# Optimization experiments

Hardware: AMD Instinct MI355X
Metric: run time of the kernel (lower is better)

Reference implementation:

```python
import jax, jax.numpy as jnp
import numpy as np

# Per-sample token counts per octree depth layer (full octree, depth 1..5)
LENS = (8, 64, 512, 4096, 32768)
OFFS = np.concatenate([[0], np.cumsum(LENS)]).astype(int)
CONV = (1, 1, 1, 4, 8)  # conv stride/kernel per layer: basic x3, half-conv (2^(3-1)), single-conv (2^3)
B, E = 8, 256
NUM_VOCAB, RES, SDIM = 16, 32, 3
S = int(OFFS[-1])  # 37448


def setup_inputs() -> dict:
    key = jax.random.key(0)
    ks = jax.random.split(key, 16)
    value = jax.random.randint(ks[0], (B, S), 1, NUM_VOCAB + 1)
    # depth: fixed sorted octree pattern, same for every sample
    depth_row = np.concatenate([np.full(l, d + 1, dtype=np.int64) for d, l in enumerate(LENS)])
    depth = jnp.broadcast_to(jnp.asarray(depth_row), (B, S))
    position = jax.random.randint(ks[1], (B, S, SDIM), 1, 2 * RES)
    sc = 0.02
    val_emb = (jax.random.normal(ks[2], (5, NUM_VOCAB + 1, E)) * sc).at[:, 0].set(0.0)
    dep_emb = (jax.random.normal(ks[3], (5, RES + 1, E)) * sc).at[:, 0].set(0.0)
    pos_emb = (jax.random.normal(ks[4], (5, SDIM, 2 * RES, E)) * sc).at[:, :, 0].set(0.0)
    conv4_w = jax.random.normal(ks[5], (E, E, 4)) * sc
    conv4_b = jax.random.normal(ks[6], (E,)) * sc
    conv8_w = jax.random.normal(ks[7], (E, E, 8)) * sc
    conv8_b = jax.random.normal(ks[8], (E,)) * sc
    return {"value": value, "depth": depth, "position": position,
            "val_emb": val_emb, "dep_emb": dep_emb, "pos_emb": pos_emb,
            "conv4_w": conv4_w, "conv4_b": conv4_b, "conv8_w": conv8_w, "conv8_b": conv8_b}


def _embed(v, d, p, ve, de, pe):
    # sum of value, depth, and per-axis spatial embeddings  [B, L, E]
    return ve[v] + de[d] + pe[0][p[:, :, 0]] + pe[1][p[:, :, 1]] + pe[2][p[:, :, 2]]


def _conv(x, w, b, s):
    # Conv1d(kernel=stride=s) == blockwise GEMM over non-overlapping windows
    Bb, L, Ee = x.shape
    xr = x.reshape(Bb, L // s, s, Ee)
    return jnp.einsum('blki,oik->blo', xr, w) + b


def reference(value, depth, position, val_emb, dep_emb, pos_emb, conv4_w, conv4_b, conv8_w, conv8_b):
    convs = {3: (conv4_w, conv4_b), 4: (conv8_w, conv8_b)}
    outs = []
    for li in range(5):
        s0, s1 = int(OFFS[li]), int(OFFS[li + 1])
        x = _embed(value[:, s0:s1], depth[:, s0:s1], position[:, s0:s1],
                   val_emb[li], dep_emb[li], pos_emb[li])
        if CONV[li] > 1:
            w, b = convs[li]
            x = _conv(x, w, b, CONV[li])
        outs.append(x)
    # all samples share the depth layout -> equal lengths, pad_sequence is a no-op concat
    return jnp.concatenate(outs, axis=1)  # [B, 5704, E]
```

## Files before the change

kernel.cpp:

```cpp
#include <hip/hip_runtime.h>
#include <hip/hip_bf16.h>

#define S_TOT 37448
#define OUT_ROWS 5704
#define EDIM 256
#define BATCH 8

typedef __attribute__((ext_vector_type(8))) short short8;
typedef __attribute__((ext_vector_type(4))) float f32x4;
typedef __attribute__((ext_vector_type(4))) unsigned int u32x4;

__device__ __forceinline__ short f2b(float f) {
    unsigned u = __builtin_bit_cast(unsigned, f);
    unsigned r = (u + 0x7fffu + ((u >> 16) & 1u)) >> 16;
    return (short)r;
}
__device__ __forceinline__ float b2f(short s) {
    unsigned u = ((unsigned)(unsigned short)s) << 16;
    return __builtin_bit_cast(float, u);
}

__device__ __forceinline__ void embed8f(const float* ve, const float* de,
                                        const float* q0, const float* q1, const float* q2,
                                        float* s) {
#pragma unroll
    for (int h = 0; h < 2; ++h) {
        f32x4 a = *(const f32x4*)(ve + h * 4);
        f32x4 b = *(const f32x4*)(de + h * 4);
        f32x4 c = *(const f32x4*)(q0 + h * 4);
        f32x4 d = *(const f32x4*)(q1 + h * 4);
        f32x4 e = *(const f32x4*)(q2 + h * 4);
#pragma unroll
        for (int j = 0; j < 4; ++j)
            s[h * 4 + j] = a[j] + b[j] + c[j] + d[j] + e[j];
    }
}

__device__ __forceinline__ void acc_bf8(float* a, short8 s) {
    u32x4 u = __builtin_bit_cast(u32x4, s);
#pragma unroll
    for (int j = 0; j < 4; ++j) {
        a[2 * j]     += __builtin_bit_cast(float, u[j] << 16);
        a[2 * j + 1] += __builtin_bit_cast(float, u[j] & 0xffff0000u);
    }
}

template <int S>
__device__ __forceinline__ void transform_body(const float* __restrict__ w,
                                               short* __restrict__ dst, int bid, int tid) {
    int idx = bid * 256 + tid;
    int l  = idx & 63;
    int nf = (idx >> 6) & 15;
    int kb = idx >> 10;
    int o = nf * 16 + (l & 15);
    int kap0 = kb * 32 + ((l >> 4) << 3);
    short8 r;
#pragma unroll
    for (int j = 0; j < 8; ++j) {
        int kap = kap0 + j;
        int kpos = kap >> 8;
        int i = kap & 255;
        r[j] = f2b(w[(o * 256 + i) * S + kpos]);
    }
    *(short8*)(dst + idx * 8) = r;
}

__global__ __launch_bounds__(256) void transform_both(
        const float* __restrict__ w4, const float* __restrict__ w8,
        short* __restrict__ wt4, short* __restrict__ wt8) {
    int bid = blockIdx.x, tid = threadIdx.x;
    if (bid < 128) transform_body<4>(w4, wt4, bid, tid);
    else           transform_body<8>(w8, wt8, bid - 128, tid);
}

template <int S>
__device__ __forceinline__ void precompute_body(
        const float* __restrict__ val_emb, const float* __restrict__ dep_emb,
        const float* __restrict__ pos_emb, const short* __restrict__ wt2,
        short* __restrict__ P, int bid, int tid, short* As) {
    constexpr int LI = (S == 4) ? 3 : 4;
    const int lane = tid & 63;
    const int wid = tid >> 6;
    const int wave_m = wid >> 1;
    const int wave_n = wid & 1;
    const int k  = bid >> 2;
    const int mt = bid & 3;

    f32x4 acc[2][8];
#pragma unroll
    for (int i = 0; i < 2; ++i)
#pragma unroll
        for (int j = 0; j < 8; ++j) acc[i][j] = (f32x4){0.f, 0.f, 0.f, 0.f};

    const int tk = tid >> 5;
    const int f0 = (tid & 31) * 8;
    const float* dep = dep_emb + (LI * 33 + LI + 1) * 256;

#pragma unroll
    for (int m8 = 0; m8 < 8; ++m8) {
        int m = m8 * 8 + tk;
        int R = mt * 64 + m;
        short8 r;
        if (R < 17) {
            const float* src = val_emb + (LI * 17 + R) * 256;
#pragma unroll
            for (int j = 0; j < 8; ++j) r[j] = f2b(src[f0 + j] + dep[f0 + j]);
        } else if (R < 209) {
            int ax = (R < 81) ? 0 : (R < 145 ? 1 : 2);
            int rr = R - (ax == 0 ? 17 : (ax == 1 ? 81 : 145));
            const float* src = pos_emb + ((LI * 3 + ax) * 64 + rr) * 256;
#pragma unroll
            for (int j = 0; j < 8; ++j) r[j] = f2b(src[f0 + j]);
        } else {
            r = (short8){0, 0, 0, 0, 0, 0, 0, 0};
        }
        int byte = (m * 512 + f0 * 2) ^ ((m & 7) << 4);
        *(short8*)((char*)As + byte) = r;
    }
    __syncthreads();

#pragma unroll
    for (int ks = 0; ks < 8; ++ks) {
        short8 af[2];
#pragma unroll
        for (int mf = 0; mf < 2; ++mf) {
            int m = wave_m * 32 + mf * 16 + (lane & 15);
            int byte = (m * 512 + ks * 64 + ((lane >> 4) << 4)) ^ ((m & 7) << 4);
            af[mf] = *(const short8*)((const char*)As + byte);
        }
        int kbg = k * 8 + ks;
#pragma unroll
        for (int nf = 0; nf < 8; ++nf) {
            int nfg = wave_n * 8 + nf;
            short8 bfr = *(const short8*)(wt2 + ((kbg * 16 + nfg) * 64 + lane) * 8);
            acc[0][nf] = __builtin_amdgcn_mfma_f32_16x16x32_bf16(af[0], bfr, acc[0][nf], 0, 0, 0);
            acc[1][nf] = __builtin_amdgcn_mfma_f32_16x16x32_bf16(af[1], bfr, acc[1][nf], 0, 0, 0);
        }
    }

#pragma unroll
    for (int mf = 0; mf < 2; ++mf) {
#pragma unroll
        for (int nf = 0; nf < 8; ++nf) {
            int n = wave_n * 128 + nf * 16 + (lane & 15);
            int r0 = mt * 64 + wave_m * 32 + mf * 16 + ((lane >> 4) << 2);
#pragma unroll
            for (int reg = 0; reg < 4; ++reg)
                P[(k * 256 + r0 + reg) * 256 + n] = f2b(acc[mf][nf][reg]);
        }
    }
}

__global__ __launch_bounds__(256) void precompute_both(
        const float* __restrict__ val_emb, const float* __restrict__ dep_emb,
        const float* __restrict__ pos_emb, const short* __restrict__ wt4,
        const short* __restrict__ wt8, short* __restrict__ P4, short* __restrict__ P8) {
    __shared__ __align__(16) short As[64 * 256];
    if (blockIdx.x < 16)
        precompute_body<4>(val_emb, dep_emb, pos_emb, wt4, P4, blockIdx.x, threadIdx.x, As);
    else
        precompute_body<8>(val_emb, dep_emb, pos_emb, wt8, P8, blockIdx.x - 16, threadIdx.x, As);
}

template <int S>
__device__ __forceinline__ void gather_body32(
        const int* __restrict__ value, const int* __restrict__ position,
        const short* __restrict__ P, const float* __restrict__ bias,
        float* __restrict__ out, int bid, int tid, int4* idx_lds) {
    constexpr int L_OUT = (S == 4) ? 1024 : 4096;
    constexpr int OFF_IN = (S == 4) ? 584 : 4680;
    constexpr int OFF_OUT = (S == 4) ? 584 : 1608;

    const int R0 = bid * 32;
    const int b = R0 / L_OUT;
    const int l0 = R0 - b * L_OUT;
    const int tbase = b * S_TOT + OFF_IN + l0 * S;

    if (tid < 32 * S) {
        int v  = value[tbase + tid];
        int p0 = position[(tbase + tid) * 3 + 0];
        int p1 = position[(tbase + tid) * 3 + 1];
        int p2 = position[(tbase + tid) * 3 + 2];
        idx_lds[tid] = make_int4(v << 8, (17 + p0) << 8,
                                 (81 + p1) << 8, (145 + p2) << 8);
    }
    __syncthreads();

    const int r = tid >> 5;
    const int og = (tid & 31) * 8;
    const short* Pg = P + og;
    f32x4 bb0 = *(const f32x4*)(bias + og);
    f32x4 bb1 = *(const f32x4*)(bias + og + 4);

    int4 id = idx_lds[r * S];
    short8 s0 = *(const short8*)(Pg + id.x);
    short8 s1 = *(const short8*)(Pg + id.y);
    short8 s2 = *(const short8*)(Pg + id.z);
    short8 s3 = *(const short8*)(Pg + id.w);

#pragma unroll
    for (int rr = 0; rr < 4; ++rr) {
        const int row = rr * 8 + r;
        float a[8];
#pragma unroll
        for (int j = 0; j < 4; ++j) { a[j] = bb0[j]; a[4 + j] = bb1[j]; }
#pragma unroll
        for (int k = 0; k < S; ++k) {
            short8 t0 = s0, t1 = s1, t2 = s2, t3 = s3;
            const bool more = !(rr == 3 && k == S - 1);
            if (more) {
                const int nk = (k + 1 < S) ? k + 1 : 0;
                const int nrow = (k + 1 < S) ? row : row + 8;
                int4 idn = idx_lds[nrow * S + nk];
                const short* Pn = Pg + (nk << 16);
                t0 = *(const short8*)(Pn + idn.x);
                t1 = *(const short8*)(Pn + idn.y);
                t2 = *(const short8*)(Pn + idn.z);
                t3 = *(const short8*)(Pn + idn.w);
            }
            acc_bf8(a, s0);
            acc_bf8(a, s1);
            acc_bf8(a, s2);
            acc_bf8(a, s3);
            s0 = t0; s1 = t1; s2 = t2; s3 = t3;
        }
        float* op = out + ((long)b * OUT_ROWS + OFF_OUT + l0 + row) * EDIM + og;
        __builtin_nontemporal_store((f32x4){a[0], a[1], a[2], a[3]}, (f32x4*)op);
        __builtin_nontemporal_store((f32x4){a[4], a[5], a[6], a[7]}, (f32x4*)(op + 4));
    }
}

__device__ __forceinline__ void embed_small_body(
        const int* __restrict__ value, const int* __restrict__ depth,
        const int* __restrict__ position, const float* __restrict__ val_emb,
        const float* __restrict__ dep_emb, const float* __restrict__ pos_emb,
        float* __restrict__ out, int bid, int tid) {
    int idx = bid * 256 + tid;
    int token = idx >> 5;
    int f0 = (idx & 31) * 8;
    int b = token / 584;
    int r = token - b * 584;
    int li = (r < 8) ? 0 : (r < 72 ? 1 : 2);
    int base = b * S_TOT + r;
    int v = value[base];
    int d = depth[base];
    const int* pp = position + base * 3;
    const float* ve = val_emb + ((li * 17 + v) << 8) + f0;
    const float* de = dep_emb + ((li * 33 + d) << 8) + f0;
    const float* q0 = pos_emb + (((li * 3 + 0) * 64 + pp[0]) << 8) + f0;
    const float* q1 = pos_emb + (((li * 3 + 1) * 64 + pp[1]) << 8) + f0;
    const float* q2 = pos_emb + (((li * 3 + 2) * 64 + pp[2]) << 8) + f0;
    float s[8];
    embed8f(ve, de, q0, q1, q2, s);
    float* op = out + ((long)b * OUT_ROWS + r) * EDIM + f0;
    *(f32x4*)op = (f32x4){s[0], s[1], s[2], s[3]};
    *(f32x4*)(op + 4) = (f32x4){s[4], s[5], s[6], s[7]};
}

__global__ __launch_bounds__(256) void gather_mega(
        const int* __restrict__ value, const int* __restrict__ depth,
        const int* __restrict__ position, const float* __restrict__ val_emb,
        const float* __restrict__ dep_emb, const float* __restrict__ pos_emb,
        const short* __restrict__ P4, const short* __restrict__ P8,
        const float* __restrict__ b4, const float* __restrict__ b8,
        float* __restrict__ out) {
    __shared__ int4 idx_lds[256];
    int bid = blockIdx.x, tid = threadIdx.x;
    if (bid < 1024)
        gather_body32<8>(value, position, P8, b8, out, bid, tid, idx_lds);
    else if (bid < 1280)
        gather_body32<4>(value, position, P4, b4, out, bid - 1024, tid, idx_lds);
    else
        embed_small_body(value, depth, position, val_emb, dep_emb, pos_emb, out, bid - 1280, tid);
}

__global__ __launch_bounds__(256) void embed_small_kernel(
        const int* __restrict__ value, const int* __restrict__ depth,
        const int* __restrict__ position, const float* __restrict__ val_emb,
        const float* __restrict__ dep_emb, const float* __restrict__ pos_emb,
        float* __restrict__ out) {
    embed_small_body(value, depth, position, val_emb, dep_emb, pos_emb, out,
                     blockIdx.x, threadIdx.x);
}

template <int S>
__global__ __launch_bounds__(256) void conv_kernel(
        const int* __restrict__ value, const int* __restrict__ depth,
        const int* __restrict__ position, const float* __restrict__ val_emb,
        const float* __restrict__ dep_emb, const float* __restrict__ pos_emb,
        const short* __restrict__ wt2, const float* __restrict__ bias,
        float* __restrict__ out) {
    constexpr int LI = (S == 4) ? 3 : 4;
    constexpr int L_OUT = (S == 4) ? 1024 : 4096;
    constexpr int OFF_IN = (S == 4) ? 584 : 4680;
    constexpr int OFF_OUT = (S == 4) ? 584 : 1608;

    __shared__ __align__(16) short As[64 * 256];

    const int tid = threadIdx.x;
    const int lane = tid & 63;
    const int wid = tid >> 6;
    const int wave_m = wid >> 1;
    const int wave_n = wid & 1;
    const int mg0 = blockIdx.x * 64;
    const int b = mg0 / L_OUT;
    const int l0 = mg0 - b * L_OUT;

    f32x4 acc[2][8];
#pragma unroll
    for (int i = 0; i < 2; ++i)
#pragma unroll
        for (int j = 0; j < 8; ++j) acc[i][j] = (f32x4){0.f, 0.f, 0.f, 0.f};

    const int tk = tid >> 5;
    const int f0 = (tid & 31) * 8;

    for (int cp = 0; cp < S; ++cp) {
        __syncthreads();
#pragma unroll
        for (int m8 = 0; m8 < 8; ++m8) {
            int m = m8 * 8 + tk;
            int t = OFF_IN + (l0 + m) * S + cp;
            int base = b * S_TOT + t;
            int v = value[base];
            int d = depth[base];
            const int* pp = position + base * 3;
            const float* ve = val_emb + ((LI * 17 + v) << 8) + f0;
            const float* de = dep_emb + ((LI * 33 + d) << 8) + f0;
            const float* q0 = pos_emb + (((LI * 3 + 0) * 64 + pp[0]) << 8) + f0;
            const float* q1 = pos_emb + (((LI * 3 + 1) * 64 + pp[1]) << 8) + f0;
            const float* q2 = pos_emb + (((LI * 3 + 2) * 64 + pp[2]) << 8) + f0;
            float s[8];
            embed8f(ve, de, q0, q1, q2, s);
            short8 r;
#pragma unroll
            for (int j = 0; j < 8; ++j) r[j] = f2b(s[j]);
            int byte = (m * 512 + f0 * 2) ^ ((m & 7) << 4);
            *(short8*)((char*)As + byte) = r;
        }
        __syncthreads();
#pragma unroll
        for (int ks = 0; ks < 8; ++ks) {
            short8 af[2];
#pragma unroll
            for (int mf = 0; mf < 2; ++mf) {
                int m = wave_m * 32 + mf * 16 + (lane & 15);
                int byte = (m * 512 + ks * 64 + ((lane >> 4) << 4)) ^ ((m & 7) << 4);
                af[mf] = *(const short8*)((const char*)As + byte);
            }
            int kbg = cp * 8 + ks;
#pragma unroll
            for (int nf = 0; nf < 8; ++nf) {
                int nfg = wave_n * 8 + nf;
                short8 bfr = *(const short8*)(wt2 + ((kbg * 16 + nfg) * 64 + lane) * 8);
                acc[0][nf] = __builtin_amdgcn_mfma_f32_16x16x32_bf16(af[0], bfr, acc[0][nf], 0, 0, 0);
                acc[1][nf] = __builtin_amdgcn_mfma_f32_16x16x32_bf16(af[1], bfr, acc[1][nf], 0, 0, 0);
            }
        }
    }

#pragma unroll
    for (int mf = 0; mf < 2; ++mf) {
#pragma unroll
        for (int nf = 0; nf < 8; ++nf) {
            int n = wave_n * 128 + nf * 16 + (lane & 15);
            float bv = bias[n];
            int r0 = l0 + wave_m * 32 + mf * 16 + ((lane >> 4) << 2);
#pragma unroll
            for (int reg = 0; reg < 4; ++reg)
                out[((long)b * OUT_ROWS + OFF_OUT + r0 + reg) * EDIM + n] =
                    acc[mf][nf][reg] + bv;
        }
    }
}

extern "C" void kernel_launch(void* const* d_in, const int* in_sizes, int n_in,
                              void* d_out, int out_size, void* d_ws, size_t ws_size,
                              hipStream_t stream) {
    const int* value = (const int*)d_in[0];
    const int* depth = (const int*)d_in[1];
    const int* position = (const int*)d_in[2];
    const float* val_emb = (const float*)d_in[3];
    const float* dep_emb = (const float*)d_in[4];
    const float* pos_emb = (const float*)d_in[5];
    const float* w4 = (const float*)d_in[6];
    const float* b4 = (const float*)d_in[7];
    const float* w8 = (const float*)d_in[8];
    const float* b8 = (const float*)d_in[9];
    float* out = (float*)d_out;

    short* wt4 = (short*)d_ws;
    short* wt8 = wt4 + 262144;
    short* P4  = (short*)((char*)d_ws + 1572864);
    short* P8  = P4 + 262144;
    const size_t need = 3145728;

    transform_both<<<dim3(384), dim3(256), 0, stream>>>(w4, w8, wt4, wt8);

    if (ws_size >= need) {
        precompute_both<<<dim3(48), dim3(256), 0, stream>>>(val_emb, dep_emb, pos_emb,
                                                            wt4, wt8, P4, P8);
        gather_mega<<<dim3(1864), dim3(256), 0, stream>>>(value, depth, position,
                                                          val_emb, dep_emb, pos_emb,
                                                          P4, P8, b4, b8, out);
    } else {
        embed_small_kernel<<<dim3(584), dim3(256), 0, stream>>>(value, depth, position,
                                                                val_emb, dep_emb, pos_emb, out);
        conv_kernel<4><<<dim3(128), dim3(256), 0, stream>>>(value, depth, position, val_emb,
                                                            dep_emb, pos_emb, wt4, b4, out);
        conv_kernel<8><<<dim3(512), dim3(256), 0, stream>>>(value, depth, position, val_emb,
                                                            dep_emb, pos_emb, wt8, b8, out);
    }
}
```

Before: 61.16 us.

## Stage precomputed projection slices in LDS and gather from shared memory

```diff
diff --git a/kernel.cpp b/kernel.cpp
--- a/kernel.cpp
+++ b/kernel.cpp
@@ -163,70 +163,72 @@
 }
 
 template <int S>
-__device__ __forceinline__ void gather_body32(
+__device__ __forceinline__ void gather_lds_body(
         const int* __restrict__ value, const int* __restrict__ position,
         const short* __restrict__ P, const float* __restrict__ bias,
-        float* __restrict__ out, int bid, int tid, int4* idx_lds) {
+        float* __restrict__ out, int bid, int tid,
+        char* Pl, unsigned* idxp) {
     constexpr int L_OUT = (S == 4) ? 1024 : 4096;
     constexpr int OFF_IN = (S == 4) ? 584 : 4680;
     constexpr int OFF_OUT = (S == 4) ? 584 : 1608;
 
-    const int R0 = bid * 32;
+    const int rc  = bid >> 2;
+    const int og0 = (bid & 3) * 64;
+    const int R0 = rc * 128;
     const int b = R0 / L_OUT;
     const int l0 = R0 - b * L_OUT;
-    const int tbase = b * S_TOT + OFF_IN + l0 * S;
-
-    if (tid < 32 * S) {
-        int v  = value[tbase + tid];
-        int p0 = position[(tbase + tid) * 3 + 0];
-        int p1 = position[(tbase + tid) * 3 + 1];
-        int p2 = position[(tbase + tid) * 3 + 2];
-        idx_lds[tid] = make_int4(v << 8, (17 + p0) << 8,
-                                 (81 + p1) << 8, (145 + p2) << 8);
-    }
-    __syncthreads();
-
-    const int r = tid >> 5;
-    const int og = (tid & 31) * 8;
-    const short* Pg = P + og;
-    f32x4 bb0 = *(const f32x4*)(bias + og);
-    f32x4 bb1 = *(const f32x4*)(bias + og + 4);
-
-    int4 id = idx_lds[r * S];
-    short8 s0 = *(const short8*)(Pg + id.x);
-    short8 s1 = *(const short8*)(Pg + id.y);
-    short8 s2 = *(const short8*)(Pg + id.z);
-    short8 s3 = *(const short8*)(Pg + id.w);
-
-#pragma unroll
-    for (int rr = 0; rr < 4; ++rr) {
-        const int row = rr * 8 + r;
-        float a[8];
-#pragma unroll
-        for (int j = 0; j < 4; ++j) { a[j] = bb0[j]; a[4 + j] = bb1[j]; }
-#pragma unroll
-        for (int k = 0; k < S; ++k) {
-            short8 t0 = s0, t1 = s1, t2 = s2, t3 = s3;
-            const bool more = !(rr == 3 && k == S - 1);
-            if (more) {
-                const int nk = (k + 1 < S) ? k + 1 : 0;
-                const int nrow = (k + 1 < S) ? row : row + 8;
-                int4 idn = idx_lds[nrow * S + nk];
-                const short* Pn = Pg + (nk << 16);
-                t0 = *(const short8*)(Pn + idn.x);
-                t1 = *(const short8*)(Pn + idn.y);
-                t2 = *(const short8*)(Pn + idn.z);
-                t3 = *(const short8*)(Pn + idn.w);
-            }
-            acc_bf8(a, s0);
-            acc_bf8(a, s1);
-            acc_bf8(a, s2);
-            acc_bf8(a, s3);
-            s0 = t0; s1 = t1; s2 = t2; s3 = t3;
-        }
-        float* op = out + ((long)b * OUT_ROWS + OFF_OUT + l0 + row) * EDIM + og;
-        __builtin_nontemporal_store((f32x4){a[0], a[1], a[2], a[3]}, (f32x4*)op);
-        __builtin_nontemporal_store((f32x4){a[4], a[5], a[6], a[7]}, (f32x4*)(op + 4));
+    const long tb = (long)b * S_TOT + OFF_IN + (long)l0 * S;
+
+    for (int t = tid; t < 128 * S; t += 256) {
+        int v = value[tb + t];
+        const int* pp = position + (tb + t) * 3;
+        idxp[t] = (unsigned)v | ((unsigned)(17 + pp[0]) << 8) |
+                  ((unsigned)(81 + pp[1]) << 16) | ((unsigned)(145 + pp[2]) << 24);
+    }
+
+    const int rg = tid >> 3;
+    const int cg = tid & 7;
+    const int ogt = og0 + cg * 8;
+    f32x4 bb0 = *(const f32x4*)(bias + ogt);
+    f32x4 bb1 = *(const f32x4*)(bias + ogt + 4);
+    float a[4][8];
+#pragma unroll
+    for (int jj = 0; jj < 4; ++jj)
+#pragma unroll
+        for (int j = 0; j < 4; ++j) { a[jj][j] = bb0[j]; a[jj][4 + j] = bb1[j]; }
+
+    const short* Ps = P + og0;
+    for (int k = 0; k < S; ++k) {
+        __syncthreads();
+#pragma unroll
+        for (int it = 0; it < 8; ++it) {
+            int c = it * 256 + tid;
+            int row = c >> 3, ch = c & 7;
+            short8 v = *(const short8*)(Ps + (k << 16) + (row << 8) + ch * 8);
+            *(short8*)(Pl + row * 144 + ch * 16) = v;
+        }
+        __syncthreads();
+#pragma unroll
+        for (int jj = 0; jj < 4; ++jj) {
+            int row = rg * 4 + jj;
+            unsigned pk = idxp[row * S + k];
+            short8 s0 = *(const short8*)(Pl + (pk & 255u) * 144 + cg * 16);
+            short8 s1 = *(const short8*)(Pl + ((pk >> 8) & 255u) * 144 + cg * 16);
+            short8 s2 = *(const short8*)(Pl + ((pk >> 16) & 255u) * 144 + cg * 16);
+            short8 s3 = *(const short8*)(Pl + (pk >> 24) * 144 + cg * 16);
+            acc_bf8(a[jj], s0);
+            acc_bf8(a[jj], s1);
+            acc_bf8(a[jj], s2);
+            acc_bf8(a[jj], s3);
+        }
+    }
+
+#pragma unroll
+    for (int jj = 0; jj < 4; ++jj) {
+        int row = rg * 4 + jj;
+        float* op = out + ((long)b * OUT_ROWS + OFF_OUT + l0 + row) * EDIM + ogt;
+        __builtin_nontemporal_store((f32x4){a[jj][0], a[jj][1], a[jj][2], a[jj][3]}, (f32x4*)op);
+        __builtin_nontemporal_store((f32x4){a[jj][4], a[jj][5], a[jj][6], a[jj][7]}, (f32x4*)(op + 4));
     }
 }
 
@@ -264,12 +266,13 @@
         const short* __restrict__ P4, const short* __restrict__ P8,
         const float* __restrict__ b4, const float* __restrict__ b8,
         float* __restrict__ out) {
-    __shared__ int4 idx_lds[256];
+    __shared__ __align__(16) char Pl[256 * 144];
+    __shared__ unsigned idxp[128 * 8];
     int bid = blockIdx.x, tid = threadIdx.x;
     if (bid < 1024)
-        gather_body32<8>(value, position, P8, b8, out, bid, tid, idx_lds);
+        gather_lds_body<8>(value, position, P8, b8, out, bid, tid, Pl, idxp);
     else if (bid < 1280)
-        gather_body32<4>(value, position, P4, b4, out, bid - 1024, tid, idx_lds);
+        gather_lds_body<4>(value, position, P4, b4, out, bid - 1024, tid, Pl, idxp);
     else
         embed_small_body(value, depth, position, val_emb, dep_emb, pos_emb, out, bid - 1280, tid);
 }
```

New measurement: 84.65 us. +38.4%, slower.

## Fuse transform, precompute and gather into one cooperative kernel with grid syncs

Applied to the files above, without the earlier changes.

```diff
diff --git a/kernel.cpp b/kernel.cpp
--- a/kernel.cpp
+++ b/kernel.cpp
@@ -1,5 +1,8 @@
 #include <hip/hip_runtime.h>
 #include <hip/hip_bf16.h>
+#include <hip/hip_cooperative_groups.h>
+
+namespace cg = cooperative_groups;
 
 #define S_TOT 37448
 #define OUT_ROWS 5704
@@ -14,10 +17,6 @@
     unsigned u = __builtin_bit_cast(unsigned, f);
     unsigned r = (u + 0x7fffu + ((u >> 16) & 1u)) >> 16;
     return (short)r;
-}
-__device__ __forceinline__ float b2f(short s) {
-    unsigned u = ((unsigned)(unsigned short)s) << 16;
-    return __builtin_bit_cast(float, u);
 }
 
 __device__ __forceinline__ void embed8f(const float* ve, const float* de,
@@ -257,6 +256,39 @@
     *(f32x4*)(op + 4) = (f32x4){s[4], s[5], s[6], s[7]};
 }
 
+__global__ __launch_bounds__(256, 5) void mega_coop(
+        const int* __restrict__ value, const int* __restrict__ depth,
+        const int* __restrict__ position, const float* __restrict__ val_emb,
+        const float* __restrict__ dep_emb, const float* __restrict__ pos_emb,
+        const float* __restrict__ w4, const float* __restrict__ b4,
+        const float* __restrict__ w8, const float* __restrict__ b8,
+        short* __restrict__ wt4, short* __restrict__ wt8,
+        short* __restrict__ P4, short* __restrict__ P8,
+        float* __restrict__ out) {
+    __shared__ __align__(16) char smem[32768];
+    cg::grid_group grid = cg::this_grid();
+    const int bid = blockIdx.x, tid = threadIdx.x;
+
+    if (bid < 128)       transform_body<4>(w4, wt4, bid, tid);
+    else if (bid < 384)  transform_body<8>(w8, wt8, bid - 128, tid);
+    else if (bid < 968)  embed_small_body(value, depth, position, val_emb, dep_emb,
+                                          pos_emb, out, bid - 384, tid);
+    __threadfence();
+    grid.sync();
+
+    if (bid < 16)
+        precompute_body<4>(val_emb, dep_emb, pos_emb, wt4, P4, bid, tid, (short*)smem);
+    else if (bid < 48)
+        precompute_body<8>(val_emb, dep_emb, pos_emb, wt8, P8, bid - 16, tid, (short*)smem);
+    __threadfence();
+    grid.sync();
+
+    if (bid < 1024)
+        gather_body32<8>(value, position, P8, b8, out, bid, tid, (int4*)smem);
+    else
+        gather_body32<4>(value, position, P4, b4, out, bid - 1024, tid, (int4*)smem);
+}
+
 __global__ __launch_bounds__(256) void gather_mega(
         const int* __restrict__ value, const int* __restrict__ depth,
         const int* __restrict__ position, const float* __restrict__ val_emb,
@@ -274,106 +306,6 @@
         embed_small_body(value, depth, position, val_emb, dep_emb, pos_emb, out, bid - 1280, tid);
 }
 
-__global__ __launch_bounds__(256) void embed_small_kernel(
-        const int* __restrict__ value, const int* __restrict__ depth,
-        const int* __restrict__ position, const float* __restrict__ val_emb,
-        const float* __restrict__ dep_emb, const float* __restrict__ pos_emb,
-        float* __restrict__ out) {
-    embed_small_body(value, depth, position, val_emb, dep_emb, pos_emb, out,
-                     blockIdx.x, threadIdx.x);
-}
-
-template <int S>
-__global__ __launch_bounds__(256) void conv_kernel(
-        const int* __restrict__ value, const int* __restrict__ depth,
-        const int* __restrict__ position, const float* __restrict__ val_emb,
-        const float* __restrict__ dep_emb, const float* __restrict__ pos_emb,
-        const short* __restrict__ wt2, const float* __restrict__ bias,
-        float* __restrict__ out) {
-    constexpr int LI = (S == 4) ? 3 : 4;
-    constexpr int L_OUT = (S == 4) ? 1024 : 4096;
-    constexpr int OFF_IN = (S == 4) ? 584 : 4680;
-    constexpr int OFF_OUT = (S == 4) ? 584 : 1608;
-
-    __shared__ __align__(16) short As[64 * 256];
-
-    const int tid = threadIdx.x;
-    const int lane = tid & 63;
-    const int wid = tid >> 6;
-    const int wave_m = wid >> 1;
-    const int wave_n = wid & 1;
-    const int mg0 = blockIdx.x * 64;
-    const int b = mg0 / L_OUT;
-    const int l0 = mg0 - b * L_OUT;
-
-    f32x4 acc[2][8];
-#pragma unroll
-    for (int i = 0; i < 2; ++i)
-#pragma unroll
-        for (int j = 0; j < 8; ++j) acc[i][j] = (f32x4){0.f, 0.f, 0.f, 0.f};
-
-    const int tk = tid >> 5;
-    const int f0 = (tid & 31) * 8;
-
-    for (int cp = 0; cp < S; ++cp) {
-        __syncthreads();
-#pragma unroll
-        for (int m8 = 0; m8 < 8; ++m8) {
-            int m = m8 * 8 + tk;
-            int t = OFF_IN + (l0 + m) * S + cp;
-            int base = b * S_TOT + t;
-            int v = value[base];
-            int d = depth[base];
-            const int* pp = position + base * 3;
-            const float* ve = val_emb + ((LI * 17 + v) << 8) + f0;
-            const float* de = dep_emb + ((LI * 33 + d) << 8) + f0;
-            const float* q0 = pos_emb + (((LI * 3 + 0) * 64 + pp[0]) << 8) + f0;
-            const float* q1 = pos_emb + (((LI * 3 + 1) * 64 + pp[1]) << 8) + f0;
-            const float* q2 = pos_emb + (((LI * 3 + 2) * 64 + pp[2]) << 8) + f0;
-            float s[8];
-            embed8f(ve, de, q0, q1, q2, s);
-            short8 r;
-#pragma unroll
-            for (int j = 0; j < 8; ++j) r[j] = f2b(s[j]);
-            int byte = (m * 512 + f0 * 2) ^ ((m & 7) << 4);
-            *(short8*)((char*)As + byte) = r;
-        }
-        __syncthreads();
-#pragma unroll
-        for (int ks = 0; ks < 8; ++ks) {
-            short8 af[2];
-#pragma unroll
-            for (int mf = 0; mf < 2; ++mf) {
-                int m = wave_m * 32 + mf * 16 + (lane & 15);
-                int byte = (m * 512 + ks * 64 + ((lane >> 4) << 4)) ^ ((m & 7) << 4);
-                af[mf] = *(const short8*)((const char*)As + byte);
-            }
-            int kbg = cp * 8 + ks;
-#pragma unroll
-            for (int nf = 0; nf < 8; ++nf) {
-                int nfg = wave_n * 8 + nf;
-                short8 bfr = *(const short8*)(wt2 + ((kbg * 16 + nfg) * 64 + lane) * 8);
-                acc[0][nf] = __builtin_amdgcn_mfma_f32_16x16x32_bf16(af[0], bfr, acc[0][nf], 0, 0, 0);
-                acc[1][nf] = __builtin_amdgcn_mfma_f32_16x16x32_bf16(af[1], bfr, acc[1][nf], 0, 0, 0);
-            }
-        }
-    }
-
-#pragma unroll
-    for (int mf = 0; mf < 2; ++mf) {
-#pragma unroll
-        for (int nf = 0; nf < 8; ++nf) {
-            int n = wave_n * 128 + nf * 16 + (lane & 15);
-            float bv = bias[n];
-            int r0 = l0 + wave_m * 32 + mf * 16 + ((lane >> 4) << 2);
-#pragma unroll
-            for (int reg = 0; reg < 4; ++reg)
-                out[((long)b * OUT_ROWS + OFF_OUT + r0 + reg) * EDIM + n] =
-                    acc[mf][nf][reg] + bv;
-        }
-    }
-}
-
 extern "C" void kernel_launch(void* const* d_in, const int* in_sizes, int n_in,
                               void* d_out, int out_size, void* d_ws, size_t ws_size,
                               hipStream_t stream) {
@@ -395,20 +327,30 @@
     short* P8  = P4 + 262144;
     const size_t need = 3145728;
 
+    bool coop = false;
+    if (ws_size >= need) {
+        int dev = 0, nCU = 0, perCU = 0;
+        if (hipGetDevice(&dev) == hipSuccess &&
+            hipDeviceGetAttribute(&nCU, hipDeviceAttributeMultiprocessorCount, dev) == hipSuccess &&
+            hipOccupancyMaxActiveBlocksPerMultiprocessor(&perCU, mega_coop, 256, 0) == hipSuccess) {
+            coop = ((long)perCU * nCU >= 1280);
+        }
+    }
+
+    if (coop) {
+        void* kargs[] = { (void*)&value, (void*)&depth, (void*)&position, (void*)&val_emb,
+                          (void*)&dep_emb, (void*)&pos_emb, (void*)&w4, (void*)&b4,
+                          (void*)&w8, (void*)&b8, (void*)&wt4, (void*)&wt8,
+                          (void*)&P4, (void*)&P8, (void*)&out };
+        hipError_t e = hipLaunchCooperativeKernel((void*)mega_coop, dim3(1280), dim3(256),
+                                                  kargs, 0, stream);
+        if (e == hipSuccess) return;
+    }
+
     transform_both<<<dim3(384), dim3(256), 0, stream>>>(w4, w8, wt4, wt8);
-
-    if (ws_size >= need) {
-        precompute_both<<<dim3(48), dim3(256), 0, stream>>>(val_emb, dep_emb, pos_emb,
-                                                            wt4, wt8, P4, P8);
-        gather_mega<<<dim3(1864), dim3(256), 0, stream>>>(value, depth, position,
-                                                          val_emb, dep_emb, pos_emb,
-                                                          P4, P8, b4, b8, out);
-    } else {
-        embed_small_kernel<<<dim3(584), dim3(256), 0, stream>>>(value, depth, position,
-                                                                val_emb, dep_emb, pos_emb, out);
-        conv_kernel<4><<<dim3(128), dim3(256), 0, stream>>>(value, depth, position, val_emb,
-                                                            dep_emb, pos_emb, wt4, b4, out);
-        conv_kernel<8><<<dim3(512), dim3(256), 0, stream>>>(value, depth, position, val_emb,
-                                                            dep_emb, pos_emb, wt8, b8, out);
-    }
-}
+    precompute_both<<<dim3(48), dim3(256), 0, stream>>>(val_emb, dep_emb, pos_emb,
+                                                        wt4, wt8, P4, P8);
+    gather_mega<<<dim3(1864), dim3(256), 0, stream>>>(value, depth, position,
+                                                      val_emb, dep_emb, pos_emb,
+                                                      P4, P8, b4, b8, out);
+}
```

Result: no change. 61.51 us (+0.6%).
